# Performance work log

Measured on AMD Instinct MI355X. Metric: run time of the kernel, lower is better.

The kernel has to match this reference:

```python
import jax, jax.numpy as jnp
import numpy as np

FEAT_STRIDE = 16
NEG_OV, POS_OV = 0.3, 0.7
RPN_BATCH = 256
NUM_FG = int(0.5 * RPN_BATCH)  # RPN_FG_FRACTION * RPN_BATCHSIZE


def _gen_anchors(base=16, ratios=(0.5, 1.0, 2.0), scales=(4, 8, 16)):
    # 3D extension of the classic generate_anchors: ratio warps w/h, scale multiplies all dims
    ctr = (base - 1) / 2.0
    rows = []
    for r in ratios:
        for s in scales:
            w = base * s * np.sqrt(1.0 / r)
            h = base * s * np.sqrt(r)
            d = float(base * s)
            rows.append([ctr - 0.5 * (w - 1), ctr - 0.5 * (h - 1),
                         ctr + 0.5 * (w - 1), ctr + 0.5 * (h - 1),
                         ctr - 0.5 * (d - 1), ctr + 0.5 * (d - 1)])
    return np.asarray(rows, np.float32)


def setup_inputs() -> dict:
    key = jax.random.key(0)
    ks = jax.random.split(key, 8)
    B, H, W, D, K, A = 2, 48, 48, 24, 20, 9
    cls = jax.random.normal(ks[0], (B, 2 * A, H, W, D), jnp.float32)
    x1 = jax.random.uniform(ks[1], (B, K)) * 600.0
    y1 = jax.random.uniform(ks[2], (B, K)) * 600.0
    z1 = jax.random.uniform(ks[3], (B, K)) * 300.0
    whd = 16.0 + jax.random.uniform(ks[4], (B, K, 3)) * jnp.array([104.0, 104.0, 48.0])
    x2 = jnp.minimum(x1 + whd[..., 0], 767.0)
    y2 = jnp.minimum(y1 + whd[..., 1], 767.0)
    z2 = jnp.minimum(z1 + whd[..., 2], 383.0)
    cid = jax.random.randint(ks[5], (B, K), 1, 4).astype(jnp.float32)
    gt_boxes = jnp.stack([x1, y1, x2, y2, z1, z2, cid], axis=2)
    im_info = jnp.tile(jnp.array([[768.0, 768.0, 384.0]], jnp.float32), (B, 1))
    total = H * W * D * A
    return {
        'rpn_cls_score': cls,
        'gt_boxes': gt_boxes,
        'im_info': im_info,
        'num_boxes': jnp.full((B,), K, jnp.int32),
        'anchors': jnp.asarray(_gen_anchors()),
        'rand_fg': jax.random.uniform(ks[6], (B, total)),
        'rand_bg': jax.random.uniform(ks[7], (B, total)),
    }


def _overlaps(anc, gt):
    # anc: (N,6) [x1,y1,x2,y2,z1,z2]; gt: (B,K,7) -> IoU (B,N,K)
    aw = anc[:, 2] - anc[:, 0] + 1.0
    ah = anc[:, 3] - anc[:, 1] + 1.0
    ad = anc[:, 5] - anc[:, 4] + 1.0
    a_area = aw * ah * ad  # (N,)
    gw = gt[:, :, 2] - gt[:, :, 0] + 1.0
    gh = gt[:, :, 3] - gt[:, :, 1] + 1.0
    gd = gt[:, :, 5] - gt[:, :, 4] + 1.0
    g_area = gw * gh * gd  # (B,K)
    iw = jnp.clip(jnp.minimum(anc[None, :, None, 2], gt[:, None, :, 2]) -
                  jnp.maximum(anc[None, :, None, 0], gt[:, None, :, 0]) + 1.0, 0.0)
    ih = jnp.clip(jnp.minimum(anc[None, :, None, 3], gt[:, None, :, 3]) -
                  jnp.maximum(anc[None, :, None, 1], gt[:, None, :, 1]) + 1.0, 0.0)
    idp = jnp.clip(jnp.minimum(anc[None, :, None, 5], gt[:, None, :, 5]) -
                   jnp.maximum(anc[None, :, None, 4], gt[:, None, :, 4]) + 1.0, 0.0)
    inter = iw * ih * idp
    ov = inter / (a_area[None, :, None] + g_area[:, None, :] - inter)
    gt_zero = (gw == 1.0) & (gh == 1.0) & (gd == 1.0)
    a_zero = (aw == 1.0) & (ah == 1.0) & (ad == 1.0)
    ov = jnp.where(gt_zero[:, None, :], 0.0, ov)
    ov = jnp.where(a_zero[None, :, None], -1.0, ov)
    return ov


def _transform(ex, gt):
    # ex: (N,6); gt: (B,N,6) -> (B,N,6) targets (dx,dy,dz,dw,dh,dd)
    ew = ex[:, 2] - ex[:, 0] + 1.0
    eh = ex[:, 3] - ex[:, 1] + 1.0
    ed = ex[:, 5] - ex[:, 4] + 1.0
    ecx = ex[:, 0] + 0.5 * (ew - 1.0)
    ecy = ex[:, 1] + 0.5 * (eh - 1.0)
    ecz = ex[:, 4] + 0.5 * (ed - 1.0)
    gw = gt[:, :, 2] - gt[:, :, 0] + 1.0
    gh = gt[:, :, 3] - gt[:, :, 1] + 1.0
    gd = gt[:, :, 5] - gt[:, :, 4] + 1.0
    gcx = gt[:, :, 0] + 0.5 * (gw - 1.0)
    gcy = gt[:, :, 1] + 0.5 * (gh - 1.0)
    gcz = gt[:, :, 4] + 0.5 * (gd - 1.0)
    return jnp.stack([(gcx - ecx[None]) / ew[None],
                      (gcy - ecy[None]) / eh[None],
                      (gcz - ecz[None]) / ed[None],
                      jnp.log(gw / ew[None]),
                      jnp.log(gh / eh[None]),
                      jnp.log(gd / ed[None])], axis=2)


def _rank(p):
    # rank of each element when sorted by descending priority, per row
    return jnp.argsort(jnp.argsort(-p, axis=1), axis=1)


def reference(rpn_cls_score, gt_boxes, im_info, num_boxes, anchors, rand_fg, rand_bg):
    B = gt_boxes.shape[0]
    H, W, D = rpn_cls_score.shape[2], rpn_cls_score.shape[3], rpn_cls_score.shape[4]
    A = anchors.shape[0]
    sx = jnp.arange(W, dtype=jnp.float32) * FEAT_STRIDE
    sy = jnp.arange(H, dtype=jnp.float32) * FEAT_STRIDE
    sz = jnp.arange(D, dtype=jnp.float32) * FEAT_STRIDE
    mx, my, mz = jnp.meshgrid(sx, sy, sz, indexing='xy')  # (H,W,D) each
    shifts = jnp.stack([mx.ravel(), my.ravel(), mx.ravel(), my.ravel(), mz.ravel(), mz.ravel()], axis=1)
    all_anchors = (anchors[None, :, :] + shifts[:, None, :]).reshape(-1, 6)  # (total,6)
    total = all_anchors.shape[0]
    inside = ((all_anchors[:, 0] >= 0) & (all_anchors[:, 1] >= 0) & (all_anchors[:, 4] >= 0) &
              (all_anchors[:, 2] < im_info[0, 1]) & (all_anchors[:, 3] < im_info[0, 0]) &
              (all_anchors[:, 5] < im_info[0, 2]))  # (total,)

    ov = _overlaps(all_anchors, gt_boxes)                       # (B,total,K)
    ov_m = jnp.where(inside[None, :, None], ov, -1.0)           # mask outside anchors
    max_ov = ov_m.max(axis=2)
    argmax_ov = jnp.argmax(ov_m, axis=2)                        # (B,total)

    labels = jnp.full((B, total), -1.0, jnp.float32)
    ins = inside[None, :]
    labels = jnp.where(ins & (max_ov < NEG_OV), 0.0, labels)
    gt_max = ov_m.max(axis=1)                                   # (B,K)
    gt_max = jnp.where(gt_max == 0.0, 1e-5, gt_max)
    tie = jnp.sum(ov_m == gt_max[:, None, :], axis=2) > 0
    labels = jnp.where(ins & tie, 1.0, labels)
    labels = jnp.where(ins & (max_ov >= POS_OV), 1.0, labels)

    # fg subsampling: randomly keep at most NUM_FG positives per image
    fg = labels == 1.0
    rk = _rank(jnp.where(fg, rand_fg, -1.0))
    labels = jnp.where(fg & (rk >= NUM_FG), -1.0, labels)
    # bg subsampling: keep RPN_BATCH - num_fg negatives per image
    num_bg = RPN_BATCH - jnp.sum(labels == 1.0, axis=1)         # (B,)
    bg = labels == 0.0
    rkb = _rank(jnp.where(bg, rand_bg, -1.0))
    labels = jnp.where(bg & (rkb >= num_bg[:, None]), -1.0, labels)

    assigned = jnp.take_along_axis(gt_boxes, argmax_ov[:, :, None], axis=1)  # (B,total,7)
    bbox_targets = _transform(all_anchors, assigned[:, :, :6])
    bbox_targets = jnp.where(inside[None, :, None], bbox_targets, 0.0)

    in_w = jnp.where(labels == 1.0, 1.0, 0.0)                   # RPN_BBOX_INSIDE_WEIGHTS[0]=1
    # replicate original bug: weights from the LAST image's example count
    num_examples = jnp.sum(labels[-1] >= 0.0).astype(jnp.float32)
    w = 1.0 / num_examples
    out_w = jnp.where(labels == 1.0, w, jnp.where(labels == 0.0, w, 0.0))

    labels_o = labels.reshape(B, H, W, D, A).transpose(0, 4, 1, 2, 3).reshape(B, 1, A * H * D, W)
    bt_o = bbox_targets.reshape(B, H, W, D, A * 6).transpose(0, 4, 1, 2, 3)
    iw_o = jnp.broadcast_to(in_w[:, :, None], (B, total, 6)).reshape(B, H, W, D, 6 * A).transpose(0, 4, 1, 2, 3)
    ow_o = jnp.broadcast_to(out_w[:, :, None], (B, total, 6)).reshape(B, H, W, D, 6 * A).transpose(0, 4, 1, 2, 3)
    return labels_o, bt_o, iw_o, ow_o
```

## Files before the change

### kernel.cpp

```cpp
#include <hip/hip_runtime.h>
#include <math.h>

#define BB 2
#define HH 48
#define WW 48
#define DD 24
#define KK 20
#define AA 9
#define TOTAL (HH*WW*DD*AA)
#define SPAT (HH*WW*DD)
#define OUT0N (BB*TOTAL)
#define CH 54
#define NB 4096
#define CAPB 256
#define FG_QUOTA 128
#define RPN_B 256
#define STRIDE_F 16.0f

#define O_REC    0
#define O_GTMAX  (OUT0N)
#define O_HIST   (O_GTMAX + BB*KK)
#define O_CUT    (O_HIST + 4*NB)
#define O_W      (O_CUT + 16)
#define O_LIST   (O_W + 1)

__device__ __forceinline__ unsigned enc_f(float f){
  unsigned u = __float_as_uint(f);
  return (u & 0x80000000u) ? ~u : (u | 0x80000000u);
}
__device__ __forceinline__ float dec_f(unsigned u){
  return (u & 0x80000000u) ? __uint_as_float(u & 0x7FFFFFFFu) : __uint_as_float(~u);
}
#define ENC_NEG1 0x407FFFFFu

__device__ __forceinline__ float iou_pre(float ax1,float ay1,float ax2,float ay2,
                                         float az1,float az2,float a_area,
                                         const float* g){
  #pragma clang fp contract(off)
  float iw = fminf(ax2,g[2]) - fmaxf(ax1,g[0]) + 1.0f; iw = fmaxf(iw,0.0f);
  float ih = fminf(ay2,g[3]) - fmaxf(ay1,g[1]) + 1.0f; ih = fmaxf(ih,0.0f);
  float id = fminf(az2,g[5]) - fmaxf(az1,g[4]) + 1.0f; id = fmaxf(id,0.0f);
  float inter = iw*ih*id;
  return inter / ((a_area + g[6]) - inter);
}

__device__ __forceinline__ void gt_derive(const float* gt7, float* g8){
  #pragma clang fp contract(off)
  float gw = gt7[2]-gt7[0]+1.0f, gh = gt7[3]-gt7[1]+1.0f, gd = gt7[5]-gt7[4]+1.0f;
  g8[0]=gt7[0]; g8[1]=gt7[1]; g8[2]=gt7[2]; g8[3]=gt7[3];
  g8[4]=gt7[4]; g8[5]=gt7[5]; g8[6]=gw*gh*gd; g8[7]=0.0f;
}

#define GM_SB 27
__global__ void __launch_bounds__(256) k_gtmax(const float* __restrict__ gt,
    const float* __restrict__ anc, const float* __restrict__ imi,
    unsigned* __restrict__ ws){
  __shared__ float s_gd[KK*8];
  __shared__ float s_a6[6];
  __shared__ float s_im[3];
  __shared__ unsigned s_max[KK];
  int tid = threadIdx.x;
  int a = blockIdx.y;
  int b = blockIdx.z;
  if (b == 0 && a == 0 && blockIdx.x < 16){
    int base = blockIdx.x*256 + tid;
    #pragma unroll
    for (int j=0;j<4;j++) ws[O_HIST + j*NB + base] = 0u;
  }
  if (tid < KK) gt_derive(&gt[(b*KK+tid)*7], &s_gd[tid*8]);
  if (tid < 6)  s_a6[tid] = anc[a*6+tid];
  if (tid < 3)  s_im[tid] = imi[tid];
  if (tid < KK) s_max[tid] = ENC_NEG1;
  __syncthreads();
  float rmax[KK];
  #pragma unroll
  for (int k=0;k<KK;k++) rmax[k] = -1.0f;
  int s0 = blockIdx.x*256 + tid;
  for (int j=0; j<8; j++){
    int s = s0 + j*(GM_SB*256);
    int d = s % DD; int s2 = s / DD;
    int w = s2 % WW; int h = s2 / WW;
    float fx = w*STRIDE_F, fy = h*STRIDE_F, fz = d*STRIDE_F;
    float ax1=s_a6[0]+fx, ay1=s_a6[1]+fy, ax2=s_a6[2]+fx;
    float ay2=s_a6[3]+fy, az1=s_a6[4]+fz, az2=s_a6[5]+fz;
    bool inside = (ax1>=0.f)&&(ay1>=0.f)&&(az1>=0.f)&&
                  (ax2<s_im[1])&&(ay2<s_im[0])&&(az2<s_im[2]);
    if (inside){
      #pragma clang fp contract(off)
      float aw = ax2-ax1+1.0f, ah = ay2-ay1+1.0f, ad = az2-az1+1.0f;
      float a_area = aw*ah*ad;
      #pragma unroll
      for (int k=0;k<KK;k++)
        rmax[k] = fmaxf(rmax[k], iou_pre(ax1,ay1,ax2,ay2,az1,az2,a_area,&s_gd[k*8]));
    }
  }
  #pragma unroll
  for (int k=0;k<KK;k++){
    float v = rmax[k];
    for (int off=32; off>0; off>>=1) v = fmaxf(v, __shfl_down(v, off, 64));
    if ((tid & 63) == 0) atomicMax(&s_max[k], enc_f(v));
  }
  __syncthreads();
  if (tid < KK) atomicMax(&ws[O_GTMAX + b*KK + tid], s_max[tid]);
}

__global__ void __launch_bounds__(256) k_label(const float* __restrict__ gt,
    const float* __restrict__ anc, const float* __restrict__ imi,
    const float* __restrict__ rfg, const float* __restrict__ rbg,
    unsigned* __restrict__ ws){
  __shared__ float s_gd[BB*KK*8];
  __shared__ float s_anc[AA*6];
  __shared__ float s_im[3];
  __shared__ float s_gm[BB*KK];
  int tid = threadIdx.x;
  if (tid < BB*KK) gt_derive(&gt[tid*7], &s_gd[tid*8]);
  for (int j=tid; j<AA*6; j+=256) s_anc[j] = anc[j];
  if (tid<3) s_im[tid] = imi[tid];
  if (tid<BB*KK){ float g = dec_f(ws[O_GTMAX+tid]); if (g==0.0f) g = 1e-5f; s_gm[tid]=g; }
  __syncthreads();
  int t = blockIdx.x*256 + tid;
  int d = t % DD; int r1 = t/DD;
  int w = r1 % WW; int r2 = r1/WW;
  int h = r2 % HH; int r3 = r2/HH;
  int a = r3 % AA; int b = r3/AA;
  int i = ((h*WW+w)*DD + d)*AA + a;
  float fx=w*STRIDE_F, fy=h*STRIDE_F, fz=d*STRIDE_F;
  float ax1=s_anc[a*6+0]+fx, ay1=s_anc[a*6+1]+fy, ax2=s_anc[a*6+2]+fx;
  float ay2=s_anc[a*6+3]+fy, az1=s_anc[a*6+4]+fz, az2=s_anc[a*6+5]+fz;
  bool inside = (ax1>=0.f)&&(ay1>=0.f)&&(az1>=0.f)&&
                (ax2<s_im[1])&&(ay2<s_im[0])&&(az2<s_im[2]);
  float L = -1.0f;
  int am = 0;
  if (inside){
    #pragma clang fp contract(off)
    float aw = ax2-ax1+1.0f, ah = ay2-ay1+1.0f, ad = az2-az1+1.0f;
    float a_area = aw*ah*ad;
    float mv = -2.0f; bool tie = false;
    #pragma unroll
    for (int k=0;k<KK;k++){
      float ov = iou_pre(ax1,ay1,ax2,ay2,az1,az2,a_area,&s_gd[(b*KK+k)*8]);
      if (ov > mv){ mv = ov; am = k; }
      tie = tie || (ov == s_gm[b*KK+k]);
    }
    if (mv < 0.3f) L = 0.0f;
    if (tie)       L = 1.0f;
    if (mv >= 0.7f) L = 1.0f;
  }
  unsigned code = (L==1.0f) ? 2u : ((L==0.0f) ? 1u : 0u);
  unsigned bucket = 0;
  if (code){
    int fl = (code==1u ? 2 : 0) + b;
    const float* ra = (code==1u) ? rbg : rfg;
    float r = ra[b*TOTAL + i];
    bucket = (unsigned)min(NB-1, (int)(r*(float)NB));
    unsigned pos = atomicAdd(&ws[O_HIST + fl*NB + bucket], 1u);
    if (pos < CAPB) ((int*)ws)[O_LIST + ((fl*NB + (int)bucket)<<8) + pos] = i;
  }
  ws[O_REC + t] = code | ((unsigned)am<<2) | (bucket<<7);
}

__global__ void __launch_bounds__(256) k_cuts(unsigned* __restrict__ ws){
  int fl = blockIdx.x; int tid = threadIdx.x;
  int b = fl & 1; int isbg = fl >> 1;
  const int CHK = NB/256;
  __shared__ unsigned ps[256];
  __shared__ unsigned s_fg;
  if (tid == 0) s_fg = 0u;
  __syncthreads();
  unsigned part = 0;
  int hi = NB - CHK*tid;
  for (int j = hi-CHK; j < hi; j++) part += ws[O_HIST + fl*NB + j];
  if (isbg){
    unsigned pf = 0;
    for (int j = tid*CHK; j < (tid+1)*CHK; j++) pf += ws[O_HIST + b*NB + j];
    atomicAdd(&s_fg, pf);
  }
  ps[tid] = part;
  __syncthreads();
  for (int off=1; off<256; off<<=1){
    unsigned v = (tid>=off) ? ps[tid-off] : 0u;
    __syncthreads();
    ps[tid] += v;
    __syncthreads();
  }
  unsigned N = ps[255];
  unsigned excl = ps[tid] - part;
  unsigned F = isbg ? s_fg : N;
  int quota = isbg ? (RPN_B - (int)min(F, (unsigned)FG_QUOTA)) : FG_QUOTA;
  if (fl == 3 && tid == 0){
    int fgk = min((int)F, FG_QUOTA);
    int bgk = min((int)N, RPN_B - fgk);
    ((float*)ws)[O_W] = 1.0f / (float)(fgk + bgk);
  }
  int* cut = (int*)&ws[O_CUT + fl*4];
  if ((int)N <= quota){
    if (tid==0){ cut[0] = -1; cut[1] = 0; cut[2] = quota; cut[3] = 0; }
    return;
  }
  unsigned cum = excl;
  for (int bk = hi-1; bk >= hi-CHK; bk--){
    unsigned c = ws[O_HIST + fl*NB + bk];
    if (c > 0u && (unsigned)(quota-1) >= cum && (unsigned)(quota-1) < cum + c){
      cut[0] = bk; cut[1] = (int)cum; cut[2] = quota; cut[3] = (int)c;
    }
    cum += c;
  }
}

__global__ void __launch_bounds__(256) k_out(const float* __restrict__ gt,
    const float* __restrict__ anc, const float* __restrict__ imi,
    const float* __restrict__ rfg, const float* __restrict__ rbg,
    float* __restrict__ out, const unsigned* __restrict__ ws){
  __shared__ float s_gt[BB*KK*7];
  __shared__ float s_anc[AA*6];
  __shared__ float s_im[3];
  __shared__ float s_w;
  int tid = threadIdx.x;
  for (int j=tid; j<BB*KK*7; j+=256) s_gt[j] = gt[j];
  for (int j=tid; j<AA*6; j+=256) s_anc[j] = anc[j];
  if (tid<3) s_im[tid] = imi[tid];
  if (tid==0) s_w = ((const float*)ws)[O_W];
  __syncthreads();
  int t = blockIdx.x*256 + tid;
  int d = t % DD; int r1=t/DD; int w=r1%WW; int r2=r1/WW;
  int h = r2 % HH; int r3=r2/HH; int a=r3%AA; int b=r3/AA;
  unsigned rec = ws[O_REC + t];
  unsigned code = rec & 3u;
  int am = (int)((rec>>2) & 31u);
  int bucket = (int)((rec>>7) & 4095u);
  float L = (code==2u) ? 1.0f : ((code==1u) ? 0.0f : -1.0f);
  if (code){
    int isbg = (code==1u);
    int fl = isbg*2 + b;
    const int* cut = (const int*)&ws[O_CUT + fl*4];
    int cutb = cut[0];
    if (cutb >= 0){
      if (bucket < cutb) L = -1.0f;
      else if (bucket == cutb){
        int rank_base = cut[1], quota = cut[2];
        int n = min(cut[3], CAPB);
        int i = ((h*WW+w)*DD + d)*AA + a;
        const float* ra = isbg ? rbg : rfg;
        float ri = ra[b*TOTAL + i];
        const int* lst = (const int*)ws + O_LIST + ((fl*NB + cutb)<<8);
        int cnt = 0;
        for (int e=0; e<n; e++){
          int j = lst[e];
          float rj = ra[b*TOTAL + j];
          cnt += (rj > ri) || (rj == ri && j < i);
        }
        if (rank_base + cnt >= quota) L = -1.0f;
      }
    }
  }
  float fx=w*STRIDE_F, fy=h*STRIDE_F, fz=d*STRIDE_F;
  float ax1=s_anc[a*6+0]+fx, ay1=s_anc[a*6+1]+fy, ax2=s_anc[a*6+2]+fx;
  float ay2=s_anc[a*6+3]+fy, az1=s_anc[a*6+4]+fz, az2=s_anc[a*6+5]+fz;
  bool inside = (ax1>=0.f)&&(ay1>=0.f)&&(az1>=0.f)&&
                (ax2<s_im[1])&&(ay2<s_im[0])&&(az2<s_im[2]);
  float bt[6] = {0.f,0.f,0.f,0.f,0.f,0.f};
  if (inside){
    const float* g = &s_gt[(b*KK + am)*7];
    float ew=ax2-ax1+1.f, eh=ay2-ay1+1.f, ed=az2-az1+1.f;
    float ecx=ax1+0.5f*(ew-1.f), ecy=ay1+0.5f*(eh-1.f), ecz=az1+0.5f*(ed-1.f);
    float gw=g[2]-g[0]+1.f, gh=g[3]-g[1]+1.f, gd=g[5]-g[4]+1.f;
    float gcx=g[0]+0.5f*(gw-1.f), gcy=g[1]+0.5f*(gh-1.f), gcz=g[4]+0.5f*(gd-1.f);
    bt[0]=(gcx-ecx)/ew; bt[1]=(gcy-ecy)/eh; bt[2]=(gcz-ecz)/ed;
    bt[3]=logf(gw/ew);  bt[4]=logf(gh/eh);  bt[5]=logf(gd/ed);
  }
  out[t] = L;
  float iwv = (L==1.0f) ? 1.0f : 0.0f;
  float owv = (L==1.0f || L==0.0f) ? s_w : 0.0f;
  int sp = (h*WW + w)*DD + d;
  float* out1 = out + OUT0N;
  float* out2 = out1 + BB*CH*SPAT;
  float* out3 = out2 + BB*CH*SPAT;
  int basech = (b*CH + a*6)*SPAT + sp;
  #pragma unroll
  for (int c=0; c<6; c++){
    int off = basech + c*SPAT;
    out1[off] = bt[c];
    out2[off] = iwv;
    out3[off] = owv;
  }
}

extern "C" void kernel_launch(void* const* d_in, const int* in_sizes, int n_in,
                              void* d_out, int out_size, void* d_ws, size_t ws_size,
                              hipStream_t stream) {
  (void)in_sizes; (void)n_in; (void)out_size; (void)ws_size;
  const float* gt  = (const float*)d_in[1];
  const float* imi = (const float*)d_in[2];
  const float* anc = (const float*)d_in[4];
  const float* rfg = (const float*)d_in[5];
  const float* rbg = (const float*)d_in[6];
  float* out = (float*)d_out;
  unsigned* ws = (unsigned*)d_ws;
  int nb = (OUT0N + 255)/256;
  hipMemsetAsync((char*)d_ws + (size_t)O_GTMAX*4, 0, BB*KK*4, stream);
  k_gtmax <<<dim3(GM_SB, AA, BB), dim3(256), 0, stream>>>(gt, anc, imi, ws);
  k_label <<<dim3(nb), dim3(256), 0, stream>>>(gt, anc, imi, rfg, rbg, ws);
  k_cuts  <<<dim3(4), dim3(256), 0, stream>>>(ws);
  k_out   <<<dim3(nb), dim3(256), 0, stream>>>(gt, anc, imi, rfg, rbg, out, ws);
}
```

Baseline: 181.6 us.

## Fuse cut computation into label kernel via last-block pattern; process four anchors per thread

The separate cut kernel is removed. The last k_label block to finish, detected with an atomic done counter and thread fences, now computes the histogram prefix sums and cut points. Each thread in k_label and k_out now handles four consecutive depth positions, so record and output stores become 128-bit vectors and anchor x/y setup is shared across them. The gt-max slots are padded to separate cache lines to reduce atomic contention. In exchange, one block runs a serial tail, and there are 4x fewer threads for the IoU-heavy labeling work.

```diff
diff --git a/kernel.cpp b/kernel.cpp
--- a/kernel.cpp
+++ b/kernel.cpp
@@ -16,10 +16,12 @@
 #define FG_QUOTA 128
 #define RPN_B 256
 #define STRIDE_F 16.0f
+#define NBLK_L 972
 
 #define O_REC    0
 #define O_GTMAX  (OUT0N)
-#define O_HIST   (O_GTMAX + BB*KK)
+#define O_DONE   (O_GTMAX + BB*KK*16)
+#define O_HIST   (O_DONE + 1)
 #define O_CUT    (O_HIST + 4*NB)
 #define O_W      (O_CUT + 16)
 #define O_LIST   (O_W + 1)
@@ -101,7 +103,7 @@
     if ((tid & 63) == 0) atomicMax(&s_max[k], enc_f(v));
   }
   __syncthreads();
-  if (tid < KK) atomicMax(&ws[O_GTMAX + b*KK + tid], s_max[tid]);
+  if (tid < KK) atomicMax(&ws[O_GTMAX + (b*KK + tid)*16], s_max[tid]);
 }
 
 __global__ void __launch_bounds__(256) k_label(const float* __restrict__ gt,
@@ -112,98 +114,118 @@
   __shared__ float s_anc[AA*6];
   __shared__ float s_im[3];
   __shared__ float s_gm[BB*KK];
+  __shared__ unsigned ps[256];
+  __shared__ unsigned s_fg;
+  __shared__ unsigned s_lastf;
   int tid = threadIdx.x;
   if (tid < BB*KK) gt_derive(&gt[tid*7], &s_gd[tid*8]);
   for (int j=tid; j<AA*6; j+=256) s_anc[j] = anc[j];
   if (tid<3) s_im[tid] = imi[tid];
-  if (tid<BB*KK){ float g = dec_f(ws[O_GTMAX+tid]); if (g==0.0f) g = 1e-5f; s_gm[tid]=g; }
-  __syncthreads();
-  int t = blockIdx.x*256 + tid;
-  int d = t % DD; int r1 = t/DD;
+  if (tid<BB*KK){
+    float g = dec_f(ws[O_GTMAX + tid*16]); if (g==0.0f) g = 1e-5f; s_gm[tid]=g;
+  }
+  __syncthreads();
+  int t0 = (blockIdx.x*256 + tid)*4;
+  int d0 = t0 % DD; int r1 = t0/DD;
   int w = r1 % WW; int r2 = r1/WW;
   int h = r2 % HH; int r3 = r2/HH;
   int a = r3 % AA; int b = r3/AA;
-  int i = ((h*WW+w)*DD + d)*AA + a;
-  float fx=w*STRIDE_F, fy=h*STRIDE_F, fz=d*STRIDE_F;
+  float fx=w*STRIDE_F, fy=h*STRIDE_F;
   float ax1=s_anc[a*6+0]+fx, ay1=s_anc[a*6+1]+fy, ax2=s_anc[a*6+2]+fx;
-  float ay2=s_anc[a*6+3]+fy, az1=s_anc[a*6+4]+fz, az2=s_anc[a*6+5]+fz;
-  bool inside = (ax1>=0.f)&&(ay1>=0.f)&&(az1>=0.f)&&
-                (ax2<s_im[1])&&(ay2<s_im[0])&&(az2<s_im[2]);
-  float L = -1.0f;
-  int am = 0;
-  if (inside){
-    #pragma clang fp contract(off)
-    float aw = ax2-ax1+1.0f, ah = ay2-ay1+1.0f, ad = az2-az1+1.0f;
-    float a_area = aw*ah*ad;
-    float mv = -2.0f; bool tie = false;
-    #pragma unroll
-    for (int k=0;k<KK;k++){
-      float ov = iou_pre(ax1,ay1,ax2,ay2,az1,az2,a_area,&s_gd[(b*KK+k)*8]);
-      if (ov > mv){ mv = ov; am = k; }
-      tie = tie || (ov == s_gm[b*KK+k]);
-    }
-    if (mv < 0.3f) L = 0.0f;
-    if (tie)       L = 1.0f;
-    if (mv >= 0.7f) L = 1.0f;
-  }
-  unsigned code = (L==1.0f) ? 2u : ((L==0.0f) ? 1u : 0u);
-  unsigned bucket = 0;
-  if (code){
-    int fl = (code==1u ? 2 : 0) + b;
-    const float* ra = (code==1u) ? rbg : rfg;
-    float r = ra[b*TOTAL + i];
-    bucket = (unsigned)min(NB-1, (int)(r*(float)NB));
-    unsigned pos = atomicAdd(&ws[O_HIST + fl*NB + bucket], 1u);
-    if (pos < CAPB) ((int*)ws)[O_LIST + ((fl*NB + (int)bucket)<<8) + pos] = i;
-  }
-  ws[O_REC + t] = code | ((unsigned)am<<2) | (bucket<<7);
-}
-
-__global__ void __launch_bounds__(256) k_cuts(unsigned* __restrict__ ws){
-  int fl = blockIdx.x; int tid = threadIdx.x;
-  int b = fl & 1; int isbg = fl >> 1;
-  const int CHK = NB/256;
-  __shared__ unsigned ps[256];
-  __shared__ unsigned s_fg;
-  if (tid == 0) s_fg = 0u;
-  __syncthreads();
-  unsigned part = 0;
-  int hi = NB - CHK*tid;
-  for (int j = hi-CHK; j < hi; j++) part += ws[O_HIST + fl*NB + j];
-  if (isbg){
-    unsigned pf = 0;
-    for (int j = tid*CHK; j < (tid+1)*CHK; j++) pf += ws[O_HIST + b*NB + j];
-    atomicAdd(&s_fg, pf);
-  }
-  ps[tid] = part;
-  __syncthreads();
-  for (int off=1; off<256; off<<=1){
-    unsigned v = (tid>=off) ? ps[tid-off] : 0u;
+  float ay2=s_anc[a*6+3]+fy;
+  bool in_xy = (ax1>=0.f)&&(ay1>=0.f)&&(ax2<s_im[1])&&(ay2<s_im[0]);
+  unsigned rec4[4];
+  for (int q=0; q<4; q++){
+    int d = d0 + q;
+    float fz = d*STRIDE_F;
+    float az1=s_anc[a*6+4]+fz, az2=s_anc[a*6+5]+fz;
+    bool inside = in_xy && (az1>=0.f) && (az2<s_im[2]);
+    float L = -1.0f;
+    int am = 0;
+    if (inside){
+      #pragma clang fp contract(off)
+      float aw = ax2-ax1+1.0f, ah = ay2-ay1+1.0f, ad = az2-az1+1.0f;
+      float a_area = aw*ah*ad;
+      float mv = -2.0f; bool tie = false;
+      #pragma unroll
+      for (int k=0;k<KK;k++){
+        float ov = iou_pre(ax1,ay1,ax2,ay2,az1,az2,a_area,&s_gd[(b*KK+k)*8]);
+        if (ov > mv){ mv = ov; am = k; }
+        tie = tie || (ov == s_gm[b*KK+k]);
+      }
+      if (mv < 0.3f) L = 0.0f;
+      if (tie)       L = 1.0f;
+      if (mv >= 0.7f) L = 1.0f;
+    }
+    unsigned code = (L==1.0f) ? 2u : ((L==0.0f) ? 1u : 0u);
+    unsigned bucket = 0;
+    if (code){
+      int i = ((h*WW+w)*DD + d)*AA + a;
+      int fl = (code==1u ? 2 : 0) + b;
+      const float* ra = (code==1u) ? rbg : rfg;
+      float r = ra[b*TOTAL + i];
+      bucket = (unsigned)min(NB-1, (int)(r*(float)NB));
+      unsigned pos = atomicAdd(&ws[O_HIST + fl*NB + bucket], 1u);
+      if (pos < CAPB) ((int*)ws)[O_LIST + ((fl*NB + (int)bucket)<<8) + pos] = i;
+    }
+    rec4[q] = code | ((unsigned)am<<2) | (bucket<<7);
+  }
+  uint4 u; u.x=rec4[0]; u.y=rec4[1]; u.z=rec4[2]; u.w=rec4[3];
+  *(uint4*)&ws[O_REC + t0] = u;
+
+  __syncthreads();
+  if (tid == 0){
+    __threadfence();
+    unsigned old = atomicAdd(&ws[O_DONE], 1u);
+    s_lastf = (old == NBLK_L - 1) ? 1u : 0u;
+  }
+  __syncthreads();
+  if (!s_lastf) return;
+  __threadfence();
+  for (int fl=0; fl<4; fl++){
+    int b2 = fl & 1; int isbg = fl >> 1;
+    if (tid == 0) s_fg = 0u;
     __syncthreads();
-    ps[tid] += v;
+    unsigned hb[16];
+    int lo = NB - 16*(tid+1);
+    unsigned part = 0;
+    for (int j=0;j<16;j++){ hb[j] = atomicAdd(&ws[O_HIST + fl*NB + lo + j], 0u); part += hb[j]; }
+    if (isbg){
+      unsigned pf = 0;
+      for (int j=0;j<16;j++) pf += atomicAdd(&ws[O_HIST + b2*NB + tid*16 + j], 0u);
+      atomicAdd(&s_fg, pf);
+    }
+    ps[tid] = part;
     __syncthreads();
-  }
-  unsigned N = ps[255];
-  unsigned excl = ps[tid] - part;
-  unsigned F = isbg ? s_fg : N;
-  int quota = isbg ? (RPN_B - (int)min(F, (unsigned)FG_QUOTA)) : FG_QUOTA;
-  if (fl == 3 && tid == 0){
-    int fgk = min((int)F, FG_QUOTA);
-    int bgk = min((int)N, RPN_B - fgk);
-    ((float*)ws)[O_W] = 1.0f / (float)(fgk + bgk);
-  }
-  int* cut = (int*)&ws[O_CUT + fl*4];
-  if ((int)N <= quota){
-    if (tid==0){ cut[0] = -1; cut[1] = 0; cut[2] = quota; cut[3] = 0; }
-    return;
-  }
-  unsigned cum = excl;
-  for (int bk = hi-1; bk >= hi-CHK; bk--){
-    unsigned c = ws[O_HIST + fl*NB + bk];
-    if (c > 0u && (unsigned)(quota-1) >= cum && (unsigned)(quota-1) < cum + c){
-      cut[0] = bk; cut[1] = (int)cum; cut[2] = quota; cut[3] = (int)c;
-    }
-    cum += c;
+    for (int off=1; off<256; off<<=1){
+      unsigned v = (tid>=off) ? ps[tid-off] : 0u;
+      __syncthreads();
+      ps[tid] += v;
+      __syncthreads();
+    }
+    unsigned N = ps[255];
+    unsigned excl = ps[tid] - part;
+    unsigned F = isbg ? s_fg : N;
+    int quota = isbg ? (RPN_B - (int)min(F, (unsigned)FG_QUOTA)) : FG_QUOTA;
+    if (fl == 3 && tid == 0){
+      int fgk = min((int)F, FG_QUOTA);
+      int bgk = min((int)N, RPN_B - fgk);
+      ((float*)ws)[O_W] = 1.0f / (float)(fgk + bgk);
+    }
+    int* cut = (int*)&ws[O_CUT + fl*4];
+    if ((int)N <= quota){
+      if (tid==0){ cut[0] = -1; cut[1] = 0; cut[2] = quota; cut[3] = 0; }
+    } else {
+      unsigned cum = excl;
+      for (int j=15; j>=0; j--){
+        unsigned c = hb[j];
+        if (c > 0u && (unsigned)(quota-1) >= cum && (unsigned)(quota-1) < cum + c){
+          cut[0] = lo+j; cut[1] = (int)cum; cut[2] = quota; cut[3] = (int)c;
+        }
+        cum += c;
+      }
+    }
+    __syncthreads();
   }
 }
 
@@ -221,67 +243,87 @@
   if (tid<3) s_im[tid] = imi[tid];
   if (tid==0) s_w = ((const float*)ws)[O_W];
   __syncthreads();
-  int t = blockIdx.x*256 + tid;
-  int d = t % DD; int r1=t/DD; int w=r1%WW; int r2=r1/WW;
-  int h = r2 % HH; int r3=r2/HH; int a=r3%AA; int b=r3/AA;
-  unsigned rec = ws[O_REC + t];
-  unsigned code = rec & 3u;
-  int am = (int)((rec>>2) & 31u);
-  int bucket = (int)((rec>>7) & 4095u);
-  float L = (code==2u) ? 1.0f : ((code==1u) ? 0.0f : -1.0f);
-  if (code){
-    int isbg = (code==1u);
-    int fl = isbg*2 + b;
-    const int* cut = (const int*)&ws[O_CUT + fl*4];
-    int cutb = cut[0];
-    if (cutb >= 0){
-      if (bucket < cutb) L = -1.0f;
-      else if (bucket == cutb){
-        int rank_base = cut[1], quota = cut[2];
-        int n = min(cut[3], CAPB);
-        int i = ((h*WW+w)*DD + d)*AA + a;
-        const float* ra = isbg ? rbg : rfg;
-        float ri = ra[b*TOTAL + i];
-        const int* lst = (const int*)ws + O_LIST + ((fl*NB + cutb)<<8);
-        int cnt = 0;
-        for (int e=0; e<n; e++){
-          int j = lst[e];
-          float rj = ra[b*TOTAL + j];
-          cnt += (rj > ri) || (rj == ri && j < i);
+  int t0 = (blockIdx.x*256 + tid)*4;
+  int d0 = t0 % DD; int r1=t0/DD;
+  int w = r1 % WW; int r2=r1/WW;
+  int h = r2 % HH; int r3=r2/HH;
+  int a = r3 % AA; int b = r3/AA;
+  uint4 ru = *(const uint4*)&ws[O_REC + t0];
+  unsigned rec4[4] = {ru.x, ru.y, ru.z, ru.w};
+  float fx=w*STRIDE_F, fy=h*STRIDE_F;
+  float ax1=s_anc[a*6+0]+fx, ay1=s_anc[a*6+1]+fy, ax2=s_anc[a*6+2]+fx;
+  float ay2=s_anc[a*6+3]+fy;
+  bool in_xy = (ax1>=0.f)&&(ay1>=0.f)&&(ax2<s_im[1])&&(ay2<s_im[0]);
+  float Lq[4];
+  float bt[4][6];
+  for (int q=0; q<4; q++){
+    int d = d0 + q;
+    unsigned rec = rec4[q];
+    unsigned code = rec & 3u;
+    int am = (int)((rec>>2) & 31u);
+    int bucket = (int)((rec>>7) & 4095u);
+    float L = (code==2u) ? 1.0f : ((code==1u) ? 0.0f : -1.0f);
+    if (code){
+      int isbg = (code==1u);
+      int fl = isbg*2 + b;
+      const int* cut = (const int*)&ws[O_CUT + fl*4];
+      int cutb = cut[0];
+      if (cutb >= 0){
+        if (bucket < cutb) L = -1.0f;
+        else if (bucket == cutb){
+          int rank_base = cut[1], quota = cut[2];
+          int n = min(cut[3], CAPB);
+          int i = ((h*WW+w)*DD + d)*AA + a;
+          const float* ra = isbg ? rbg : rfg;
+          float ri = ra[b*TOTAL + i];
+          const int* lst = (const int*)ws + O_LIST + ((fl*NB + cutb)<<8);
+          int cnt = 0;
+          for (int e=0; e<n; e++){
+            int j = lst[e];
+            float rj = ra[b*TOTAL + j];
+            cnt += (rj > ri) || (rj == ri && j < i);
+          }
+          if (rank_base + cnt >= quota) L = -1.0f;
         }
-        if (rank_base + cnt >= quota) L = -1.0f;
       }
     }
-  }
-  float fx=w*STRIDE_F, fy=h*STRIDE_F, fz=d*STRIDE_F;
-  float ax1=s_anc[a*6+0]+fx, ay1=s_anc[a*6+1]+fy, ax2=s_anc[a*6+2]+fx;
-  float ay2=s_anc[a*6+3]+fy, az1=s_anc[a*6+4]+fz, az2=s_anc[a*6+5]+fz;
-  bool inside = (ax1>=0.f)&&(ay1>=0.f)&&(az1>=0.f)&&
-                (ax2<s_im[1])&&(ay2<s_im[0])&&(az2<s_im[2]);
-  float bt[6] = {0.f,0.f,0.f,0.f,0.f,0.f};
-  if (inside){
-    const float* g = &s_gt[(b*KK + am)*7];
-    float ew=ax2-ax1+1.f, eh=ay2-ay1+1.f, ed=az2-az1+1.f;
-    float ecx=ax1+0.5f*(ew-1.f), ecy=ay1+0.5f*(eh-1.f), ecz=az1+0.5f*(ed-1.f);
-    float gw=g[2]-g[0]+1.f, gh=g[3]-g[1]+1.f, gd=g[5]-g[4]+1.f;
-    float gcx=g[0]+0.5f*(gw-1.f), gcy=g[1]+0.5f*(gh-1.f), gcz=g[4]+0.5f*(gd-1.f);
-    bt[0]=(gcx-ecx)/ew; bt[1]=(gcy-ecy)/eh; bt[2]=(gcz-ecz)/ed;
-    bt[3]=logf(gw/ew);  bt[4]=logf(gh/eh);  bt[5]=logf(gd/ed);
-  }
-  out[t] = L;
-  float iwv = (L==1.0f) ? 1.0f : 0.0f;
-  float owv = (L==1.0f || L==0.0f) ? s_w : 0.0f;
-  int sp = (h*WW + w)*DD + d;
+    Lq[q] = L;
+    float fz = d*STRIDE_F;
+    float az1=s_anc[a*6+4]+fz, az2=s_anc[a*6+5]+fz;
+    bool inside = in_xy && (az1>=0.f) && (az2<s_im[2]);
+    if (inside){
+      const float* g = &s_gt[(b*KK + am)*7];
+      float ew=ax2-ax1+1.f, eh=ay2-ay1+1.f, ed=az2-az1+1.f;
+      float ecx=ax1+0.5f*(ew-1.f), ecy=ay1+0.5f*(eh-1.f), ecz=az1+0.5f*(ed-1.f);
+      float gw=g[2]-g[0]+1.f, gh=g[3]-g[1]+1.f, gd=g[5]-g[4]+1.f;
+      float gcx=g[0]+0.5f*(gw-1.f), gcy=g[1]+0.5f*(gh-1.f), gcz=g[4]+0.5f*(gd-1.f);
+      bt[q][0]=(gcx-ecx)/ew; bt[q][1]=(gcy-ecy)/eh; bt[q][2]=(gcz-ecz)/ed;
+      bt[q][3]=logf(gw/ew);  bt[q][4]=logf(gh/eh);  bt[q][5]=logf(gd/ed);
+    } else {
+      #pragma unroll
+      for (int c=0;c<6;c++) bt[q][c] = 0.f;
+    }
+  }
+  *(float4*)&out[t0] = make_float4(Lq[0],Lq[1],Lq[2],Lq[3]);
+  float iw0 = (Lq[0]==1.0f)?1.f:0.f, iw1 = (Lq[1]==1.0f)?1.f:0.f;
+  float iw2 = (Lq[2]==1.0f)?1.f:0.f, iw3 = (Lq[3]==1.0f)?1.f:0.f;
+  float ow0 = (Lq[0]==1.0f||Lq[0]==0.0f)?s_w:0.f;
+  float ow1 = (Lq[1]==1.0f||Lq[1]==0.0f)?s_w:0.f;
+  float ow2 = (Lq[2]==1.0f||Lq[2]==0.0f)?s_w:0.f;
+  float ow3 = (Lq[3]==1.0f||Lq[3]==0.0f)?s_w:0.f;
+  int sp0 = (h*WW + w)*DD + d0;
   float* out1 = out + OUT0N;
   float* out2 = out1 + BB*CH*SPAT;
   float* out3 = out2 + BB*CH*SPAT;
-  int basech = (b*CH + a*6)*SPAT + sp;
+  int basech = (b*CH + a*6)*SPAT + sp0;
+  float4 iwv = make_float4(iw0,iw1,iw2,iw3);
+  float4 owv = make_float4(ow0,ow1,ow2,ow3);
   #pragma unroll
   for (int c=0; c<6; c++){
     int off = basech + c*SPAT;
-    out1[off] = bt[c];
-    out2[off] = iwv;
-    out3[off] = owv;
+    *(float4*)&out1[off] = make_float4(bt[0][c],bt[1][c],bt[2][c],bt[3][c]);
+    *(float4*)&out2[off] = iwv;
+    *(float4*)&out3[off] = owv;
   }
 }
 
@@ -296,10 +338,8 @@
   const float* rbg = (const float*)d_in[6];
   float* out = (float*)d_out;
   unsigned* ws = (unsigned*)d_ws;
-  int nb = (OUT0N + 255)/256;
-  hipMemsetAsync((char*)d_ws + (size_t)O_GTMAX*4, 0, BB*KK*4, stream);
+  hipMemsetAsync((char*)d_ws + (size_t)O_GTMAX*4, 0, (BB*KK*16 + 1)*4, stream);
   k_gtmax <<<dim3(GM_SB, AA, BB), dim3(256), 0, stream>>>(gt, anc, imi, ws);
-  k_label <<<dim3(nb), dim3(256), 0, stream>>>(gt, anc, imi, rfg, rbg, ws);
-  k_cuts  <<<dim3(4), dim3(256), 0, stream>>>(ws);
-  k_out   <<<dim3(nb), dim3(256), 0, stream>>>(gt, anc, imi, rfg, rbg, out, ws);
-}
+  k_label <<<dim3(NBLK_L), dim3(256), 0, stream>>>(gt, anc, imi, rfg, rbg, ws);
+  k_out   <<<dim3(NBLK_L), dim3(256), 0, stream>>>(gt, anc, imi, rfg, rbg, out, ws);
+}
```

Result: slower. 224.8 us (+23.8%).
